# Optimization experiments

Hardware: AMD Instinct MI355X
Metric: run time of the kernel (lower is better)

## Reference

```python
import jax, jax.numpy as jnp
import numpy as np

NEG_SLOPE = 0.2  # PyG GATConv default negative_slope
EPS = 1e-16


def gat_conv(x, src, dst, num_nodes, W, a_src, a_dst, bias, heads, out_c, concat):
    """PyG-style GATConv (eval mode, self-loops already appended).
    x: [N, F_in]; src/dst: [E] (edge j->i with src=j, dst=i).
    W: [F_in, heads*out_c]; a_src/a_dst: [heads, out_c]; bias: [heads*out_c] or [out_c].
    """
    xw = (x @ W).reshape(num_nodes, heads, out_c)          # [N, H, C]
    alpha_src = jnp.sum(xw * a_src, axis=-1)               # [N, H]
    alpha_dst = jnp.sum(xw * a_dst, axis=-1)               # [N, H]
    e = jax.nn.leaky_relu(alpha_src[src] + alpha_dst[dst], NEG_SLOPE)  # [E, H]
    # numerically stable segment softmax over edges grouped by destination node
    m = jax.ops.segment_max(e, dst, num_segments=num_nodes)            # [N, H]
    e = jnp.exp(e - m[dst])
    denom = jax.ops.segment_sum(e, dst, num_segments=num_nodes)        # [N, H]
    alpha = e / (denom[dst] + EPS)                                     # [E, H]
    # weighted scatter-sum aggregation of source messages
    out = jax.ops.segment_sum(xw[src] * alpha[:, :, None], dst, num_segments=num_nodes)  # [N, H, C]
    if concat:
        out = out.reshape(num_nodes, heads * out_c)
    else:
        out = out.mean(axis=1)
    return out + bias


def setup_inputs() -> dict:
    key = jax.random.key(0)
    ks = jax.random.split(key, 12)
    N, E = 50000, 800000
    F_in, Hid, H1, Out = 512, 32, 8, 64

    def xavier(k, shape, gain=1.414):
        fan_in, fan_out = shape[0], shape[-1] if len(shape) == 2 else int(np.prod(shape[1:]))
        a = gain * np.sqrt(6.0 / (fan_in + fan_out))
        return jax.random.uniform(k, shape, jnp.float32, -a, a)

    x = jax.random.normal(ks[0], (N, F_in), jnp.float32)
    edge_index = jax.random.randint(ks[1], (2, E), 0, N, jnp.int64)

    W1 = xavier(ks[2], (F_in, H1 * Hid))
    a_src1 = xavier(ks[3], (H1, Hid))
    a_dst1 = xavier(ks[4], (H1, Hid))
    b1 = jnp.zeros((H1 * Hid,), jnp.float32)

    W2 = xavier(ks[5], (H1 * Hid, Out))
    a_src2 = xavier(ks[6], (1, Out))
    a_dst2 = xavier(ks[7], (1, Out))
    b2 = jnp.zeros((Out,), jnp.float32)

    return {"x": x, "edge_index": edge_index,
            "W1": W1, "a_src1": a_src1, "a_dst1": a_dst1, "b1": b1,
            "W2": W2, "a_src2": a_src2, "a_dst2": a_dst2, "b2": b2}


def reference(x, edge_index, W1, a_src1, a_dst1, b1, W2, a_src2, a_dst2, b2):
    N = x.shape[0]
    # add self-loops (PyG GATConv default add_self_loops=True)
    loop = jnp.arange(N, dtype=edge_index.dtype)
    src = jnp.concatenate([edge_index[0], loop])
    dst = jnp.concatenate([edge_index[1], loop])

    # eval mode: all dropouts are identity
    h = gat_conv(x, src, dst, N, W1, a_src1, a_dst1, b1, heads=8, out_c=32, concat=True)
    h = jax.nn.elu(h)
    h = gat_conv(h, src, dst, N, W2, a_src2, a_dst2, b2, heads=1, out_c=64, concat=False)
    return jax.nn.log_softmax(h, axis=1)
```

## Files before the change

kernel.cpp:

```cpp
#include <hip/hip_runtime.h>
#include <hip/hip_bf16.h>


typedef __attribute__((ext_vector_type(8)))  __bf16          bf16x8;
typedef __attribute__((ext_vector_type(8)))  unsigned short  ushort8;
typedef __attribute__((ext_vector_type(16))) float           f32x16;
typedef __attribute__((ext_vector_type(2)))  float           f32x2;

#define NEG_SLOPE 0.2f
#define EPS_GAT 1e-16f

static __device__ __forceinline__ float lrelu(float x) {
    return x > 0.0f ? x : NEG_SLOPE * x;
}
static __device__ __forceinline__ unsigned short f2bf(float f) {
    unsigned u = __float_as_uint(f);
    return (unsigned short)((u + 0x7fffu + ((u >> 16) & 1u)) >> 16);
}
static __device__ __forceinline__ float bf2f(unsigned short v) {
    return __uint_as_float(((unsigned)v) << 16);
}
static __device__ __forceinline__ unsigned encf(float x) {
    unsigned u = __float_as_uint(x);
    return (u >> 31) ? ~u : (u | 0x80000000u);
}
static __device__ __forceinline__ float decf(unsigned e) {
    unsigned u = (e >> 31) ? (e & 0x7fffffffu) : ~e;
    return __uint_as_float(u);
}

__global__ void k_hist_w(const void* __restrict__ eix, int* __restrict__ counts,
                         int E, int EB,
                         const float* __restrict__ W1, const float* __restrict__ W2,
                         unsigned short* __restrict__ w1t, unsigned short* __restrict__ w2t) {
    int b = blockIdx.x;
    if (b < EB) {
        int i = b * 256 + threadIdx.x;
        unsigned w = ((const unsigned*)eix)[2 * min(i, E - 1) + 1];
        bool is64 = (__syncthreads_or((int)(w != 0u)) == 0);
        if (i < E) {
            int d = is64 ? (int)((const long long*)eix)[E + i]
                         : ((const int*)eix)[E + i];
            atomicAdd(&counts[d], 1);
        }
    } else {
        int t = (b - EB) * 256 + threadIdx.x;
        if (t < 512 * 256) {
            int k = t >> 8, m = t & 255;
            w1t[m * 512 + k] = f2bf(W1[t]);
        } else {
            int u = t - 512 * 256;
            if (u < 256 * 64) {
                int k = u >> 6, m = u & 63;
                w2t[m * 256 + k] = f2bf(W2[u]);
            }
        }
    }
}

__global__ void k_scan1(const int* __restrict__ counts, int* __restrict__ rowp,
                        int* __restrict__ bsum, int N) {
    __shared__ int s[256];
    int t = threadIdx.x, i = blockIdx.x * 256 + t;
    int v = (i < N) ? counts[i] : 0;
    s[t] = v;
    __syncthreads();
    for (int off = 1; off < 256; off <<= 1) {
        int u = (t >= off) ? s[t - off] : 0;
        __syncthreads();
        s[t] += u;
        __syncthreads();
    }
    if (i < N) rowp[i] = s[t] - v;
    if (t == 255) bsum[blockIdx.x] = s[255];
}

__global__ void k_scan2(const int* __restrict__ bsum, int* __restrict__ boff,
                        int* __restrict__ rowp_last, int NB) {
    __shared__ int s[256];
    int t = threadIdx.x;
    int v = (t < NB) ? bsum[t] : 0;
    s[t] = v;
    __syncthreads();
    for (int off = 1; off < 256; off <<= 1) {
        int u = (t >= off) ? s[t - off] : 0;
        __syncthreads();
        s[t] += u;
        __syncthreads();
    }
    if (t < NB) boff[t] = s[t] - v;
    if (t == 255) *rowp_last = s[255];
}

__global__ void k_scan3(int* __restrict__ rowp, int* __restrict__ cursor,
                        const int* __restrict__ boff, int N) {
    int i = blockIdx.x * 256 + threadIdx.x;
    if (i < N) {
        int r = rowp[i] + boff[blockIdx.x];
        rowp[i] = r;
        cursor[i] = r;
    }
}

__global__ void k_fill(const void* __restrict__ eix, int* __restrict__ cursor,
                       int* __restrict__ ssrc, int E) {
    int i = blockIdx.x * 256 + threadIdx.x;
    unsigned w = ((const unsigned*)eix)[2 * min(i, E - 1) + 1];
    bool is64 = (__syncthreads_or((int)(w != 0u)) == 0);
    if (i >= E) return;
    int s, d;
    if (is64) {
        s = (int)((const long long*)eix)[i];
        d = (int)((const long long*)eix)[E + i];
    } else {
        s = ((const int*)eix)[i];
        d = ((const int*)eix)[E + i];
    }
    int pos = atomicAdd(&cursor[d], 1);
    ssrc[pos] = s;
}

template <int BM, int BN, int NT, bool AF32, bool OUTBF>
__global__ __launch_bounds__(NT) void k_gemm(const void* __restrict__ Ain,
                                             const unsigned short* __restrict__ Bt,
                                             void* __restrict__ Cout, int Nrows, int K) {
    constexpr int LD = 40;
    __shared__ __align__(16) unsigned short As[BM * LD];
    __shared__ __align__(16) unsigned short Bs[BN * LD];
    const int tid = threadIdx.x;
    const int blockRow = blockIdx.x * BM;
    const int wave = tid >> 6, lane = tid & 63;
    constexpr int WR = BM / 64;
    const int wr = wave % WR, wc = wave / WR;
    const int m = lane & 31;
    const int ksel = (lane >> 5) * 8;

    f32x16 acc00{}, acc01{}, acc10{}, acc11{};

    for (int kt = 0; kt < K; kt += 32) {
        if constexpr (AF32) {
            const float* A = (const float*)Ain;
            for (int idx = tid; idx < BM * 4; idx += NT) {
                int r = idx >> 2, kc = (idx & 3) * 8;
                int grow = blockRow + r;
                union { ushort8 u; __hip_bfloat162 h[4]; } cv;
                if (grow < Nrows) {
                    const float* ap = A + (size_t)grow * K + kt + kc;
                    float4 x0 = *(const float4*)ap;
                    float4 x1 = *(const float4*)(ap + 4);
                    cv.h[0] = __float22bfloat162_rn(make_float2(x0.x, x0.y));
                    cv.h[1] = __float22bfloat162_rn(make_float2(x0.z, x0.w));
                    cv.h[2] = __float22bfloat162_rn(make_float2(x1.x, x1.y));
                    cv.h[3] = __float22bfloat162_rn(make_float2(x1.z, x1.w));
                } else {
                    cv.u = ushort8{};
                }
                *(ushort8*)&As[r * LD + kc] = cv.u;
            }
        } else {
            const unsigned short* A = (const unsigned short*)Ain;
            for (int idx = tid; idx < BM * 4; idx += NT) {
                int r = idx >> 2, kc = (idx & 3) * 8;
                int grow = blockRow + r;
                ushort8 o{};
                if (grow < Nrows) o = *(const ushort8*)(A + (size_t)grow * K + kt + kc);
                *(ushort8*)&As[r * LD + kc] = o;
            }
        }
        for (int idx = tid; idx < BN * 4; idx += NT) {
            int r = idx >> 2, kc = (idx & 3) * 8;
            *(ushort8*)&Bs[r * LD + kc] = *(const ushort8*)(Bt + (size_t)r * K + kt + kc);
        }
        __syncthreads();

        #pragma unroll
        for (int kk = 0; kk < 32; kk += 16) {
            bf16x8 a0 = *(const bf16x8*)&As[(wr * 64 +      m) * LD + kk + ksel];
            bf16x8 a1 = *(const bf16x8*)&As[(wr * 64 + 32 + m) * LD + kk + ksel];
            bf16x8 b0 = *(const bf16x8*)&Bs[(wc * 64 +      m) * LD + kk + ksel];
            bf16x8 b1 = *(const bf16x8*)&Bs[(wc * 64 + 32 + m) * LD + kk + ksel];
            acc00 = __builtin_amdgcn_mfma_f32_32x32x16_bf16(a0, b0, acc00, 0, 0, 0);
            acc01 = __builtin_amdgcn_mfma_f32_32x32x16_bf16(a0, b1, acc01, 0, 0, 0);
            acc10 = __builtin_amdgcn_mfma_f32_32x32x16_bf16(a1, b0, acc10, 0, 0, 0);
            acc11 = __builtin_amdgcn_mfma_f32_32x32x16_bf16(a1, b1, acc11, 0, 0, 0);
        }
        __syncthreads();
    }

    const int dcol = wc * 64 + (lane & 31);
    const int dquad = 4 * (lane >> 5);
    auto store_tile = [&](const f32x16& a, int rt, int ct) {
        #pragma unroll
        for (int r = 0; r < 16; ++r) {
            int row = blockRow + wr * 64 + rt * 32 + (r & 3) + 8 * (r >> 2) + dquad;
            if (row < Nrows) {
                size_t off = (size_t)row * BN + dcol + ct * 32;
                if constexpr (OUTBF) ((unsigned short*)Cout)[off] = f2bf(a[r]);
                else                 ((float*)Cout)[off] = a[r];
            }
        }
    };
    store_tile(acc00, 0, 0); store_tile(acc01, 0, 1);
    store_tile(acc10, 1, 0); store_tile(acc11, 1, 1);
}

__global__ void k_alpha(const unsigned short* __restrict__ xw, const float* __restrict__ a_s,
                        const float* __restrict__ a_d, float* __restrict__ os,
                        float* __restrict__ od, unsigned* __restrict__ Menc,
                        int NH, int H, int C) {
    __shared__ float red[256];
    int t = blockIdx.x * 256 + threadIdx.x;
    float s = -1e30f, d = 0.f;
    if (t < NH) {
        int n = t / H, h = t - n * H;
        const unsigned short* row = xw + (size_t)n * H * C + h * C;
        s = 0.f;
        for (int c = 0; c < C; c += 8) {
            ushort8 v = *(const ushort8*)(row + c);
            #pragma unroll
            for (int q = 0; q < 8; ++q) {
                float f = bf2f(v[q]);
                s += f * a_s[h * C + c + q];
                d += f * a_d[h * C + c + q];
            }
        }
        os[t] = s; od[t] = d;
    }
    red[threadIdx.x] = s;
    __syncthreads();
    for (int off = 128; off >= H; off >>= 1) {
        if (threadIdx.x < off) red[threadIdx.x] = fmaxf(red[threadIdx.x], red[threadIdx.x + off]);
        __syncthreads();
    }
    if ((int)threadIdx.x < H) atomicMax(&Menc[threadIdx.x], encf(red[threadIdx.x]));
}

__global__ __launch_bounds__(256, 6) void k_agg_l1(
        const unsigned short* __restrict__ xw1, const float* __restrict__ asrc,
        const float* __restrict__ adst, const unsigned* __restrict__ Menc,
        const float* __restrict__ b1, const int* __restrict__ rp,
        const int* __restrict__ ssrc, unsigned short* __restrict__ hbf, int N) {
    int wid = (blockIdx.x * 256 + threadIdx.x) >> 6;
    if (wid >= N) return;
    const int lane = threadIdx.x & 63;
    const int g  = lane >> 4;
    const int q  = lane & 15;
    const int f0 = q * 16;
    const int h  = q >> 1;
    const int ih = wid * 8 + h;
    const float ad = adst[ih];
    const float m  = lrelu(decf(Menc[h]) + ad);
    f32x2 acc[8];
    float s;
    {
        float w = (g == 0) ? __expf(lrelu(asrc[ih] + ad) - m) : 0.0f;
        const unsigned short* pr = xw1 + (size_t)wid * 256 + f0;
        ushort8 lo = *(const ushort8*)pr;
        ushort8 hi = *(const ushort8*)(pr + 8);
        s = w;
        const unsigned* dl = (const unsigned*)&lo;
        const unsigned* dh = (const unsigned*)&hi;
        #pragma unroll
        for (int p = 0; p < 4; ++p) {
            acc[p].x     = w * __uint_as_float(dl[p] << 16);
            acc[p].y     = w * __uint_as_float(dl[p] & 0xffff0000u);
            acc[4 + p].x = w * __uint_as_float(dh[p] << 16);
            acc[4 + p].y = w * __uint_as_float(dh[p] & 0xffff0000u);
        }
    }
    const int e0 = rp[wid], e1 = rp[wid + 1];
    if (e0 < e1) {
        const int NQ = (e1 - e0 + 3) >> 2;

        auto LDJ = [&](int base, int& j, bool& v) {
            v = base + g < e1;
            j = ssrc[min(base + g, e1 - 1)];
        };
        auto LDD = [&](int j, float& as, ushort8& lo, ushort8& hi) {
            as = asrc[j * 8 + h];
            const unsigned short* p = xw1 + ((size_t)j << 8) + f0;
            lo = *(const ushort8*)p;
            hi = *(const ushort8*)(p + 8);
        };
        auto CONS = [&](bool v, float as, const ushort8& lo, const ushort8& hi) {
            float w = v ? __expf(lrelu(as + ad) - m) : 0.0f;
            s += w;
            f32x2 wp; wp.x = w; wp.y = w;
            const unsigned* dl = (const unsigned*)&lo;
            const unsigned* dh = (const unsigned*)&hi;
            #pragma unroll
            for (int p = 0; p < 4; ++p) {
                f32x2 x;
                x.x = __uint_as_float(dl[p] << 16);
                x.y = __uint_as_float(dl[p] & 0xffff0000u);
                asm("v_pk_fma_f32 %0, %1, %2, %3"
                    : "=v"(acc[p]) : "v"(x), "v"(wp), "v"(acc[p]));
            }
            #pragma unroll
            for (int p = 0; p < 4; ++p) {
                f32x2 x;
                x.x = __uint_as_float(dh[p] << 16);
                x.y = __uint_as_float(dh[p] & 0xffff0000u);
                asm("v_pk_fma_f32 %0, %1, %2, %3"
                    : "=v"(acc[4 + p]) : "v"(x), "v"(wp), "v"(acc[4 + p]));
            }
        };

        int j0, j1, j2, j3; bool v0, v1, v2, v3;
        float as0, as1; ushort8 lo0, hi0, lo1, hi1;
        LDJ(e0,      j0, v0);
        LDJ(e0 + 4,  j1, v1);
        LDD(j0, as0, lo0, hi0);
        LDJ(e0 + 8,  j2, v2);
        LDD(j1, as1, lo1, hi1);
        LDJ(e0 + 12, j3, v3);

        #pragma unroll 2
        for (int k = 0; k < NQ - 2; ++k) {
            int jN; bool vN;
            LDJ(e0 + 4 * k + 16, jN, vN);
            float as2; ushort8 lo2, hi2;
            LDD(j2, as2, lo2, hi2);
            CONS(v0, as0, lo0, hi0);
            v0 = v1; as0 = as1; lo0 = lo1; hi0 = hi1;
            v1 = v2; as1 = as2; lo1 = lo2; hi1 = hi2;
            v2 = v3; j2 = j3;
            v3 = vN; j3 = jN;
        }
        CONS(v0, as0, lo0, hi0);
        if (NQ >= 2) CONS(v1, as1, lo1, hi1);
    }
    s += __shfl_xor(s, 16, 64);
    s += __shfl_xor(s, 32, 64);
    #pragma unroll
    for (int p = 0; p < 8; ++p) {
        acc[p].x += __shfl_xor(acc[p].x, 16, 64);
        acc[p].x += __shfl_xor(acc[p].x, 32, 64);
        acc[p].y += __shfl_xor(acc[p].y, 16, 64);
        acc[p].y += __shfl_xor(acc[p].y, 32, 64);
    }
    float inv = 1.0f / (s + EPS_GAT);
    f32x2 p0 = (g & 2) ? ((g & 1) ? acc[6] : acc[4]) : ((g & 1) ? acc[2] : acc[0]);
    f32x2 p1 = (g & 2) ? ((g & 1) ? acc[7] : acc[5]) : ((g & 1) ? acc[3] : acc[1]);
    int fw = f0 + g * 4;
    float vv[4] = { p0.x, p0.y, p1.x, p1.y };
    ushort4 o;
    #pragma unroll
    for (int i = 0; i < 4; ++i) {
        float v = vv[i] * inv + b1[fw + i];
        v = v > 0.f ? v : expm1f(v);
        ((unsigned short*)&o)[i] = f2bf(v);
    }
    *(ushort4*)(hbf + (size_t)wid * 256 + fw) = o;
}

__global__ __launch_bounds__(256, 6) void k_agg_l2(
        const unsigned short* __restrict__ xw2, const float* __restrict__ asrc,
        const float* __restrict__ adst, const unsigned* __restrict__ Menc,
        const float* __restrict__ b2, const int* __restrict__ rp,
        const int* __restrict__ ssrc, float* __restrict__ out, int N) {
    int wid = (blockIdx.x * 256 + threadIdx.x) >> 6;
    if (wid >= N) return;
    const int lane = threadIdx.x & 63;
    const int g  = lane >> 3;
    const int q  = lane & 7;
    const int f0 = q * 8;
    const float ad = adst[wid];
    const float m = lrelu(decf(Menc[0]) + ad);
    f32x2 acc[4];
    float s;
    {
        float w = (g == 0) ? __expf(lrelu(asrc[wid] + ad) - m) : 0.0f;
        ushort8 xv = *(const ushort8*)(xw2 + (size_t)wid * 64 + f0);
        s = w;
        const unsigned* dx = (const unsigned*)&xv;
        #pragma unroll
        for (int p = 0; p < 4; ++p) {
            acc[p].x = w * __uint_as_float(dx[p] << 16);
            acc[p].y = w * __uint_as_float(dx[p] & 0xffff0000u);
        }
    }
    const int e0 = rp[wid], e1 = rp[wid + 1];
    if (e0 < e1) {
        const int NQ = (e1 - e0 + 7) >> 3;

        auto LDJ = [&](int base, int& j, bool& v) {
            v = base + g < e1;
            j = ssrc[min(base + g, e1 - 1)];
        };
        auto LDD = [&](int j, float& as, ushort8& xv) {
            as = asrc[j];
            xv = *(const ushort8*)(xw2 + ((size_t)j << 6) + f0);
        };
        auto CONS = [&](bool v, float as, const ushort8& xv) {
            float w = v ? __expf(lrelu(as + ad) - m) : 0.0f;
            s += w;
            f32x2 wp; wp.x = w; wp.y = w;
            const unsigned* dx = (const unsigned*)&xv;
            #pragma unroll
            for (int p = 0; p < 4; ++p) {
                f32x2 x;
                x.x = __uint_as_float(dx[p] << 16);
                x.y = __uint_as_float(dx[p] & 0xffff0000u);
                asm("v_pk_fma_f32 %0, %1, %2, %3"
                    : "=v"(acc[p]) : "v"(x), "v"(wp), "v"(acc[p]));
            }
        };

        int j0, j1, j2, j3; bool v0, v1, v2, v3;
        float as0, as1; ushort8 xv0, xv1;
        LDJ(e0,      j0, v0);
        LDJ(e0 + 8,  j1, v1);
        LDD(j0, as0, xv0);
        LDJ(e0 + 16, j2, v2);
        LDD(j1, as1, xv1);
        LDJ(e0 + 24, j3, v3);

        #pragma unroll 2
        for (int k = 0; k < NQ - 2; ++k) {
            int jN; bool vN;
            LDJ(e0 + 8 * k + 32, jN, vN);
            float as2; ushort8 xv2;
            LDD(j2, as2, xv2);
            CONS(v0, as0, xv0);
            v0 = v1; as0 = as1; xv0 = xv1;
            v1 = v2; as1 = as2; xv1 = xv2;
            v2 = v3; j2 = j3;
            v3 = vN; j3 = jN;
        }
        CONS(v0, as0, xv0);
        if (NQ >= 2) CONS(v1, as1, xv1);
    }
    s += __shfl_xor(s, 8, 64);
    s += __shfl_xor(s, 16, 64);
    s += __shfl_xor(s, 32, 64);
    #pragma unroll
    for (int p = 0; p < 4; ++p) {
        acc[p].x += __shfl_xor(acc[p].x, 8, 64);
        acc[p].x += __shfl_xor(acc[p].x, 16, 64);
        acc[p].x += __shfl_xor(acc[p].x, 32, 64);
        acc[p].y += __shfl_xor(acc[p].y, 8, 64);
        acc[p].y += __shfl_xor(acc[p].y, 16, 64);
        acc[p].y += __shfl_xor(acc[p].y, 32, 64);
    }
    float inv = 1.0f / (s + EPS_GAT);
    float val[8];
    float mx = -1e30f;
    #pragma unroll
    for (int i = 0; i < 8; ++i) {
        float a = (i & 1) ? acc[i >> 1].y : acc[i >> 1].x;
        val[i] = a * inv + b2[f0 + i];
        mx = fmaxf(mx, val[i]);
    }
    #pragma unroll
    for (int off = 4; off > 0; off >>= 1) mx = fmaxf(mx, __shfl_xor(mx, off, 64));
    float sm = 0.f;
    #pragma unroll
    for (int i = 0; i < 8; ++i) sm += __expf(val[i] - mx);
    #pragma unroll
    for (int off = 4; off > 0; off >>= 1) sm += __shfl_xor(sm, off, 64);
    float lse = mx + logf(sm);
    if (g == 0) {
        float4 o0 = make_float4(val[0] - lse, val[1] - lse, val[2] - lse, val[3] - lse);
        float4 o1 = make_float4(val[4] - lse, val[5] - lse, val[6] - lse, val[7] - lse);
        *(float4*)(out + (size_t)wid * 64 + f0)     = o0;
        *(float4*)(out + (size_t)wid * 64 + f0 + 4) = o1;
    }
}

static inline int cdiv(int a, int b) { return (a + b - 1) / b; }

extern "C" void kernel_launch(void* const* d_in, const int* in_sizes, int n_in,
                              void* d_out, int out_size, void* d_ws, size_t ws_size,
                              hipStream_t stream) {
    const float* x   = (const float*)d_in[0];
    const void*  eix = d_in[1];
    const float* W1  = (const float*)d_in[2];
    const float* as1 = (const float*)d_in[3];
    const float* ad1 = (const float*)d_in[4];
    const float* b1  = (const float*)d_in[5];
    const float* W2  = (const float*)d_in[6];
    const float* as2 = (const float*)d_in[7];
    const float* ad2 = (const float*)d_in[8];
    const float* b2  = (const float*)d_in[9];
    float* out = (float*)d_out;

    const int N = in_sizes[0] / 512;
    const int E = in_sizes[1] / 2;
    const int EB = cdiv(E, 256);
    const int WB = cdiv(512 * 256 + 256 * 64, 256);
    const int NB = cdiv(N, 256);
    const int NB1 = cdiv(N * 8, 256);
    const int NB2 = cdiv(N, 256);
    (void)n_in; (void)out_size; (void)ws_size;

    char* base = (char*)d_ws;
    size_t o = 0;
    auto alloc = [&](size_t bytes) -> char* {
        o = (o + 255) & ~(size_t)255;
        char* p = base + o;
        o += bytes;
        return p;
    };
    unsigned short* xw1b  = (unsigned short*)alloc((size_t)N * 256 * 2);
    unsigned short* hbf   = (unsigned short*)alloc((size_t)N * 256 * 2);
    unsigned short* xw2b  = (unsigned short*)alloc((size_t)N * 64 * 2);
    float*          asrc1 = (float*)alloc((size_t)N * 8 * 4);
    float*          adst1 = (float*)alloc((size_t)N * 8 * 4);
    float*          asrc2 = (float*)alloc((size_t)N * 4);
    float*          adst2 = (float*)alloc((size_t)N * 4);
    size_t zero_begin = (o + 255) & ~(size_t)255;
    unsigned*       Menc  = (unsigned*)alloc(16 * 4);
    int*            counts= (int*)alloc((size_t)N * 4);
    size_t zero_end = o;
    int*            cursor= (int*)alloc((size_t)N * 4);
    int*            rowp  = (int*)alloc((size_t)(N + 1) * 4);
    int*            bsum  = (int*)alloc(256 * 4);
    int*            boff  = (int*)alloc(256 * 4);
    unsigned short* w1t   = (unsigned short*)alloc(512 * 256 * 2);
    unsigned short* w2t   = (unsigned short*)alloc(256 * 64 * 2);
    int*            ssrc  = (int*)alloc((size_t)E * 4);

    hipMemsetAsync(base + zero_begin, 0, zero_end - zero_begin, stream);

    k_hist_w<<<EB + WB, 256, 0, stream>>>(eix, counts, E, EB, W1, W2, w1t, w2t);
    k_scan1<<<NB, 256, 0, stream>>>(counts, rowp, bsum, N);
    k_scan2<<<1, 256, 0, stream>>>(bsum, boff, rowp + N, NB);
    k_scan3<<<NB, 256, 0, stream>>>(rowp, cursor, boff, N);
    k_fill<<<EB, 256, 0, stream>>>(eix, cursor, ssrc, E);

    k_gemm<64, 256, 256, true, true><<<cdiv(N, 64), 256, 0, stream>>>(x, w1t, xw1b, N, 512);
    k_alpha<<<NB1, 256, 0, stream>>>(xw1b, as1, ad1, asrc1, adst1, Menc, N * 8, 8, 32);
    k_agg_l1<<<cdiv(N * 64, 256), 256, 0, stream>>>(xw1b, asrc1, adst1, Menc, b1,
                                                    rowp, ssrc, hbf, N);
    k_gemm<64, 64, 64, false, true><<<cdiv(N, 64), 64, 0, stream>>>(hbf, w2t, xw2b, N, 256);
    k_alpha<<<NB2, 256, 0, stream>>>(xw2b, as2, ad2, asrc2, adst2, Menc + 8, N, 1, 64);
    k_agg_l2<<<cdiv(N * 64, 256), 256, 0, stream>>>(xw2b, asrc2, adst2, Menc + 8, b2,
                                                    rowp, ssrc, out, N);
}
```

Measured before the change: 456.2 us.

## Prefetch next GEMM K-tile into registers and enlarge GEMM block tiles

The GEMM kernel now loads the next K-slice of A and B from global memory into registers while the MFMA work on the current slice runs, then writes it to shared memory at the start of the next iteration. This is meant to hide global-load latency behind compute. Both GEMM launches also use larger row tiles with more threads per block (128x256 with 512 threads, 256x64 with 256 threads), which reuses each B tile across more rows. The cost is more register pressure from the staging arrays and fewer blocks in flight.

```diff
diff --git a/kernel.cpp b/kernel.cpp
--- a/kernel.cpp
+++ b/kernel.cpp
@@ -125,6 +125,8 @@
                                              const unsigned short* __restrict__ Bt,
                                              void* __restrict__ Cout, int Nrows, int K) {
     constexpr int LD = 40;
+    constexpr int AIT = BM * 4 / NT;
+    constexpr int BIT = BN * 4 / NT;
     __shared__ __align__(16) unsigned short As[BM * LD];
     __shared__ __align__(16) unsigned short Bs[BN * LD];
     const int tid = threadIdx.x;
@@ -137,42 +139,75 @@
 
     f32x16 acc00{}, acc01{}, acc10{}, acc11{};
 
-    for (int kt = 0; kt < K; kt += 32) {
-        if constexpr (AF32) {
-            const float* A = (const float*)Ain;
-            for (int idx = tid; idx < BM * 4; idx += NT) {
-                int r = idx >> 2, kc = (idx & 3) * 8;
-                int grow = blockRow + r;
-                union { ushort8 u; __hip_bfloat162 h[4]; } cv;
+    float4  af0[AIT], af1[AIT];
+    ushort8 ab[AIT];
+    ushort8 bb[BIT];
+
+    auto loadA = [&](int kt) {
+        #pragma unroll
+        for (int i = 0; i < AIT; ++i) {
+            int idx = tid + i * NT;
+            int r = idx >> 2, kc = (idx & 3) * 8;
+            int grow = blockRow + r;
+            if constexpr (AF32) {
+                const float* A = (const float*)Ain;
                 if (grow < Nrows) {
                     const float* ap = A + (size_t)grow * K + kt + kc;
-                    float4 x0 = *(const float4*)ap;
-                    float4 x1 = *(const float4*)(ap + 4);
-                    cv.h[0] = __float22bfloat162_rn(make_float2(x0.x, x0.y));
-                    cv.h[1] = __float22bfloat162_rn(make_float2(x0.z, x0.w));
-                    cv.h[2] = __float22bfloat162_rn(make_float2(x1.x, x1.y));
-                    cv.h[3] = __float22bfloat162_rn(make_float2(x1.z, x1.w));
+                    af0[i] = *(const float4*)ap;
+                    af1[i] = *(const float4*)(ap + 4);
                 } else {
-                    cv.u = ushort8{};
+                    af0[i] = make_float4(0.f, 0.f, 0.f, 0.f);
+                    af1[i] = make_float4(0.f, 0.f, 0.f, 0.f);
                 }
-                *(ushort8*)&As[r * LD + kc] = cv.u;
-            }
-        } else {
-            const unsigned short* A = (const unsigned short*)Ain;
-            for (int idx = tid; idx < BM * 4; idx += NT) {
-                int r = idx >> 2, kc = (idx & 3) * 8;
-                int grow = blockRow + r;
+            } else {
+                const unsigned short* A = (const unsigned short*)Ain;
                 ushort8 o{};
                 if (grow < Nrows) o = *(const ushort8*)(A + (size_t)grow * K + kt + kc);
-                *(ushort8*)&As[r * LD + kc] = o;
-            }
-        }
-        for (int idx = tid; idx < BN * 4; idx += NT) {
+                ab[i] = o;
+            }
+        }
+    };
+    auto loadB = [&](int kt) {
+        #pragma unroll
+        for (int i = 0; i < BIT; ++i) {
+            int idx = tid + i * NT;
             int r = idx >> 2, kc = (idx & 3) * 8;
-            *(ushort8*)&Bs[r * LD + kc] = *(const ushort8*)(Bt + (size_t)r * K + kt + kc);
-        }
-        __syncthreads();
-
+            bb[i] = *(const ushort8*)(Bt + (size_t)r * K + kt + kc);
+        }
+    };
+    auto writeAB = [&]() {
+        #pragma unroll
+        for (int i = 0; i < AIT; ++i) {
+            int idx = tid + i * NT;
+            int r = idx >> 2, kc = (idx & 3) * 8;
+            if constexpr (AF32) {
+                union { ushort8 u; __hip_bfloat162 h[4]; } cv;
+                cv.h[0] = __float22bfloat162_rn(make_float2(af0[i].x, af0[i].y));
+                cv.h[1] = __float22bfloat162_rn(make_float2(af0[i].z, af0[i].w));
+                cv.h[2] = __float22bfloat162_rn(make_float2(af1[i].x, af1[i].y));
+                cv.h[3] = __float22bfloat162_rn(make_float2(af1[i].z, af1[i].w));
+                *(ushort8*)&As[r * LD + kc] = cv.u;
+            } else {
+                *(ushort8*)&As[r * LD + kc] = ab[i];
+            }
+        }
+        #pragma unroll
+        for (int i = 0; i < BIT; ++i) {
+            int idx = tid + i * NT;
+            int r = idx >> 2, kc = (idx & 3) * 8;
+            *(ushort8*)&Bs[r * LD + kc] = bb[i];
+        }
+    };
+
+    loadA(0);
+    loadB(0);
+    for (int kt = 0; kt < K; kt += 32) {
+        writeAB();
+        __syncthreads();
+        if (kt + 32 < K) {
+            loadA(kt + 32);
+            loadB(kt + 32);
+        }
         #pragma unroll
         for (int kk = 0; kk < 32; kk += 16) {
             bf16x8 a0 = *(const bf16x8*)&As[(wr * 64 +      m) * LD + kk + ksel];
@@ -529,11 +564,11 @@
     k_scan3<<<NB, 256, 0, stream>>>(rowp, cursor, boff, N);
     k_fill<<<EB, 256, 0, stream>>>(eix, cursor, ssrc, E);
 
-    k_gemm<64, 256, 256, true, true><<<cdiv(N, 64), 256, 0, stream>>>(x, w1t, xw1b, N, 512);
+    k_gemm<128, 256, 512, true, true><<<cdiv(N, 128), 512, 0, stream>>>(x, w1t, xw1b, N, 512);
     k_alpha<<<NB1, 256, 0, stream>>>(xw1b, as1, ad1, asrc1, adst1, Menc, N * 8, 8, 32);
     k_agg_l1<<<cdiv(N * 64, 256), 256, 0, stream>>>(xw1b, asrc1, adst1, Menc, b1,
                                                     rowp, ssrc, hbf, N);
-    k_gemm<64, 64, 64, false, true><<<cdiv(N, 64), 64, 0, stream>>>(hbf, w2t, xw2b, N, 256);
+    k_gemm<256, 64, 256, false, true><<<cdiv(N, 256), 256, 0, stream>>>(hbf, w2t, xw2b, N, 256);
     k_alpha<<<NB2, 256, 0, stream>>>(xw2b, as2, ad2, asrc2, adst2, Menc + 8, N, 1, 64);
     k_agg_l2<<<cdiv(N * 64, 256), 256, 0, stream>>>(xw2b, asrc2, adst2, Menc + 8, b2,
                                                     rowp, ssrc, out, N);
```

After: 416.7 us. -8.7%, faster.
